# Performance work log

Hardware: AMD Instinct MI355X
Metric: run time of the kernel (lower is better)

Reference implementation:

```python
import jax, jax.numpy as jnp
import numpy as np

# --- placement constants (mirror init_kwargs) ---
N = 500_000           # total nodes
M = 450_000           # movable nodes (first M)
NBX = 1024
NBY = 1024
XL = 0.0
YL = 0.0
BSX = 1.0
BSY = 1.0
K = 8                 # max bin span per axis for 'large' nodes (node size < 7*bin)


def setup_inputs() -> dict:
    key = jax.random.key(0)
    k1, k2, k3, k4, k5, k6 = jax.random.split(key, 6)
    # node centers strictly inside the die so large-node windows stay in range
    px = jax.random.uniform(k1, (N,), jnp.float32, 4.0, 1020.0)
    py = jax.random.uniform(k2, (N,), jnp.float32, 4.0, 1020.0)
    pos = jnp.concatenate([px, py])                      # [2N]
    potential_field = jax.random.normal(k3, (NBX, NBY), jnp.float32)
    rho_current = jax.random.uniform(k4, (NBX, NBY), jnp.float32, 0.1, 2.0)
    node_size_x = jax.random.uniform(k5, (N,), jnp.float32, 0.2, 6.0)
    node_size_y = jax.random.uniform(k6, (N,), jnp.float32, 0.2, 6.0)
    return {"pos": pos, "potential_field": potential_field,
            "rho_current": rho_current,
            "node_size_x": node_size_x, "node_size_y": node_size_y}


def _velocity_field(pot, hx, hy):
    # v = -grad(phi): 2nd-order central interior, 1st-order one-sided edges
    vx = -jnp.concatenate([(pot[1:2] - pot[0:1]) / hx,
                           (pot[2:] - pot[:-2]) / (2.0 * hx),
                           (pot[-1:] - pot[-2:-1]) / hx], axis=0)
    vy = -jnp.concatenate([(pot[:, 1:2] - pot[:, 0:1]) / hy,
                           (pot[:, 2:] - pot[:, :-2]) / (2.0 * hy),
                           (pot[:, -1:] - pot[:, -2:-1]) / hy], axis=1)
    return vx, vy


def _axis_window(center, size, lo, bs, nb):
    # per-node K-bin window of overlap lengths along one axis
    left = center - 0.5 * size
    right = center + 0.5 * size
    bmin = jnp.clip(jnp.floor((left - lo) / bs).astype(jnp.int32), 0, nb - 1)
    bmax = jnp.clip(jnp.floor((right - lo) / bs).astype(jnp.int32), 0, nb - 1)
    b = bmin[:, None] + jnp.arange(K, dtype=jnp.int32)        # [M,K]
    bin_left = lo + b.astype(jnp.float32) * bs
    ov = jnp.minimum(right[:, None], bin_left + bs) - jnp.maximum(left[:, None], bin_left)
    ov = jnp.where((b <= bmax[:, None]) & (ov > 0.0), ov, 0.0)
    return jnp.clip(b, 0, nb - 1), ov


def _interpolate_flux(pos, flux_x, flux_y, nsx, nsy):
    pos_x = pos[:N]
    pos_y = pos[N:]
    px = pos_x[:M]
    py = pos_y[:M]
    # --- bilinear path (small nodes) ---
    gx = (px - XL) / BSX
    gy = (py - YL) / BSY
    ix = jnp.clip(jnp.floor(gx).astype(jnp.int32), 0, NBX - 1)
    iy = jnp.clip(jnp.floor(gy).astype(jnp.int32), 0, NBY - 1)
    wx = jnp.clip(gx - ix.astype(jnp.float32), 0.0, 1.0)
    wy = jnp.clip(gy - iy.astype(jnp.float32), 0.0, 1.0)
    ix1 = jnp.clip(ix + 1, 0, NBX - 1)
    iy1 = jnp.clip(iy + 1, 0, NBY - 1)

    def bilerp(f):
        return ((1.0 - wx) * (1.0 - wy) * f[ix, iy] + wx * (1.0 - wy) * f[ix1, iy]
                + (1.0 - wx) * wy * f[ix, iy1] + wx * wy * f[ix1, iy1])

    bil_fx = bilerp(flux_x)
    bil_fy = bilerp(flux_y)
    # --- exact area-weighted path (large nodes), vectorized over K x K window ---
    w = nsx[:M]
    h = nsy[:M]
    bx, ox = _axis_window(px, w, XL, BSX, NBX)                # [M,K]
    by, oy = _axis_window(py, h, YL, BSY, NBY)                # [M,K]
    weights = ox[:, :, None] * oy[:, None, :]                 # [M,K,K] overlap areas
    fx_win = flux_x[bx[:, :, None], by[:, None, :]]           # [M,K,K]
    fy_win = flux_y[bx[:, :, None], by[:, None, :]]
    area = w * h
    safe_area = jnp.maximum(area, 1e-30)
    area_fx = jnp.where(area > 0.0, (fx_win * weights).sum((1, 2)) / safe_area, 0.0)
    area_fy = jnp.where(area > 0.0, (fy_win * weights).sum((1, 2)) / safe_area, 0.0)
    large = (w >= BSX) | (h >= BSY)
    gpx = jnp.where(large, area_fx, bil_fx)
    gpy = jnp.where(large, area_fy, bil_fy)
    grad_pos = jnp.zeros_like(pos)
    grad_pos = grad_pos.at[:M].set(gpx)
    grad_pos = grad_pos.at[N:N + M].set(gpy)
    return grad_pos


def reference(pos, potential_field, rho_current, node_size_x, node_size_y):
    vx, vy = _velocity_field(potential_field, BSX, BSY)
    bin_area = BSX * BSY
    energy = 0.5 * (rho_current * bin_area * (vx * vx + vy * vy)).sum().reshape(1)
    grad_pos = _interpolate_flux(pos, vx, vy, node_size_x, node_size_y)
    return energy, grad_pos
```

## Files before the change

### kernel.cpp

```cpp
#include <hip/hip_runtime.h>
#include <hip/hip_fp16.h>

#define NPART 500000
#define MPART 450000
#define NBXC 1024
#define NBYC 1024
#define KWIN 8

__global__ __launch_bounds__(256) void field_kernel(const float* __restrict__ pot,
                                                    const float* __restrict__ rho,
                                                    __half2* __restrict__ v,
                                                    float* __restrict__ partials) {
    const int idx = blockIdx.x * 256 + threadIdx.x;
    const int i = idx >> 10;
    const int j = idx & 1023;

    float a, b, scale;
    if (i == 0)            { a = pot[1 * NBYC + j];        b = pot[0 * NBYC + j];        scale = 1.0f; }
    else if (i == NBXC - 1){ a = pot[(NBXC-1) * NBYC + j]; b = pot[(NBXC-2) * NBYC + j]; scale = 1.0f; }
    else                   { a = pot[(i+1) * NBYC + j];    b = pot[(i-1) * NBYC + j];    scale = 0.5f; }
    const float vx = -(a - b) * scale;

    if (j == 0)            { a = pot[i * NBYC + 1];        b = pot[i * NBYC + 0];        scale = 1.0f; }
    else if (j == NBYC - 1){ a = pot[i * NBYC + NBYC-1];   b = pot[i * NBYC + NBYC-2];   scale = 1.0f; }
    else                   { a = pot[i * NBYC + j + 1];    b = pot[i * NBYC + j - 1];    scale = 0.5f; }
    const float vy = -(a - b) * scale;

    v[idx] = __floats2half2_rn(vx, vy);

    float e = rho[idx] * (vx * vx + vy * vy);
    #pragma unroll
    for (int off = 32; off > 0; off >>= 1) e += __shfl_down(e, off, 64);
    __shared__ float smem[4];
    const int lane = threadIdx.x & 63;
    const int wid  = threadIdx.x >> 6;
    if (lane == 0) smem[wid] = e;
    __syncthreads();
    if (threadIdx.x == 0) partials[blockIdx.x] = (smem[0] + smem[1]) + (smem[2] + smem[3]);
}

__global__ __launch_bounds__(1024) void reduce_kernel(const float* __restrict__ partials,
                                                      float* __restrict__ out) {
    const int t = threadIdx.x;
    float e = (partials[t] + partials[t + 1024]) + (partials[t + 2048] + partials[t + 3072]);
    #pragma unroll
    for (int off = 32; off > 0; off >>= 1) e += __shfl_down(e, off, 64);
    __shared__ float smem[16];
    const int lane = t & 63;
    const int wid  = t >> 6;
    if (lane == 0) smem[wid] = e;
    __syncthreads();
    if (t == 0) {
        float s = 0.0f;
        #pragma unroll
        for (int k = 0; k < 16; ++k) s += smem[k];
        out[0] = 0.5f * s;
    }
}

__global__ __launch_bounds__(256) void particle_kernel(const float* __restrict__ pos,
                                                       const float* __restrict__ nsx,
                                                       const float* __restrict__ nsy,
                                                       const __half2* __restrict__ v,
                                                       float* __restrict__ out) {
    const int i = blockIdx.x * 256 + threadIdx.x;
    if (i >= NPART) return;
    if (i >= MPART) {
        out[1 + i]         = 0.0f;
        out[1 + NPART + i] = 0.0f;
        return;
    }

    const float px = pos[i];
    const float py = pos[NPART + i];
    const float w  = nsx[i];
    const float h  = nsy[i];

    float gpx, gpy;
    const bool large = (w >= 1.0f) || (h >= 1.0f);
    if (!large) {
        int ix = min(max((int)floorf(px), 0), NBXC - 1);
        int iy = min(max((int)floorf(py), 0), NBYC - 1);
        const float wx = fminf(fmaxf(px - (float)ix, 0.0f), 1.0f);
        const float wy = fminf(fmaxf(py - (float)iy, 0.0f), 1.0f);
        const int ix1 = min(ix + 1, NBXC - 1);
        const int iy1 = min(iy + 1, NBYC - 1);
        const float2 f00 = __half22float2(v[ix  * NBYC + iy ]);
        const float2 f10 = __half22float2(v[ix1 * NBYC + iy ]);
        const float2 f01 = __half22float2(v[ix  * NBYC + iy1]);
        const float2 f11 = __half22float2(v[ix1 * NBYC + iy1]);
        const float w00 = (1.0f - wx) * (1.0f - wy);
        const float w10 = wx * (1.0f - wy);
        const float w01 = (1.0f - wx) * wy;
        const float w11 = wx * wy;
        gpx = w00 * f00.x + w10 * f10.x + w01 * f01.x + w11 * f11.x;
        gpy = w00 * f00.y + w10 * f10.y + w01 * f01.y + w11 * f11.y;
    } else {
        const float lx = px - 0.5f * w, rx = px + 0.5f * w;
        const float ly = py - 0.5f * h, ry = py + 0.5f * h;
        const int bminx = min(max((int)floorf(lx), 0), NBXC - 1);
        const int bmaxx = min(max((int)floorf(rx), 0), NBXC - 1);
        const int bminy = min(max((int)floorf(ly), 0), NBYC - 1);
        const int bmaxy = min(max((int)floorf(ry), 0), NBYC - 1);
        const int by0   = bminy & ~3;

        float oy[12];
        #pragma unroll
        for (int k = 0; k < 12; ++k) {
            const int b = by0 + k;
            const float bl = (float)b;
            float ov = fminf(ry, bl + 1.0f) - fmaxf(ly, bl);
            oy[k] = (b <= bmaxy && ov > 0.0f) ? ov : 0.0f;
        }

        float afx = 0.0f, afy = 0.0f;
        #pragma unroll
        for (int kx = 0; kx < KWIN; ++kx) {
            const int b = bminx + kx;
            const float bl = (float)b;
            float ov = fminf(rx, bl + 1.0f) - fmaxf(lx, bl);
            ov = (b <= bmaxx && ov > 0.0f) ? ov : 0.0f;
            if (ov == 0.0f) continue;
            const int bx = min(b, NBXC - 1);
            const float4* rp = reinterpret_cast<const float4*>(v + bx * NBYC + by0);
            float4 q0 = rp[0], q1 = rp[1], q2 = rp[2];
            const float* qs0 = &q0.x;
            const float* qs1 = &q1.x;
            const float* qs2 = &q2.x;
            float sx = 0.0f, sy = 0.0f;
            #pragma unroll
            for (int k = 0; k < 4; ++k) {
                const float2 f = __half22float2(__builtin_bit_cast(__half2, qs0[k]));
                sx += f.x * oy[k];
                sy += f.y * oy[k];
            }
            #pragma unroll
            for (int k = 0; k < 4; ++k) {
                const float2 f = __half22float2(__builtin_bit_cast(__half2, qs1[k]));
                sx += f.x * oy[4 + k];
                sy += f.y * oy[4 + k];
            }
            #pragma unroll
            for (int k = 0; k < 4; ++k) {
                const float2 f = __half22float2(__builtin_bit_cast(__half2, qs2[k]));
                sx += f.x * oy[8 + k];
                sy += f.y * oy[8 + k];
            }
            afx += sx * ov;
            afy += sy * ov;
        }
        const float inv = 1.0f / fmaxf(w * h, 1e-30f);
        gpx = afx * inv;
        gpy = afy * inv;
    }
    out[1 + i]         = gpx;
    out[1 + NPART + i] = gpy;
}

extern "C" void kernel_launch(void* const* d_in, const int* in_sizes, int n_in,
                              void* d_out, int out_size, void* d_ws, size_t ws_size,
                              hipStream_t stream) {
    const float* pos = (const float*)d_in[0];
    const float* pot = (const float*)d_in[1];
    const float* rho = (const float*)d_in[2];
    const float* nsx = (const float*)d_in[3];
    const float* nsy = (const float*)d_in[4];
    float* out = (float*)d_out;

    __half2* v      = (__half2*)d_ws;
    float* partials = (float*)((char*)d_ws + (size_t)NBXC * NBYC * sizeof(__half2));

    field_kernel<<<(NBXC * NBYC) / 256, 256, 0, stream>>>(pot, rho, v, partials);
    reduce_kernel<<<1, 1024, 0, stream>>>(partials, out);
    particle_kernel<<<(NPART + 255) / 256, 256, 0, stream>>>(pos, nsx, nsy, v, out);
}
```

Measured before the change: 33.65 us.

## Vectorize field kernel four-wide and fold energy reduction into particle kernel

Each field-kernel thread now handles four consecutive bins using float4 loads of the potential and rho rows and a single float4 store of the packed half2 velocities, cutting the thread count and partial sums by a factor of four. The separate reduce kernel is dropped; an extra block appended to the particle kernel sums the 1024 partials, saving one launch. In the large-node path the x-axis overlaps are precomputed and the per-column early-continue is removed, so all eight rows are loaded unconditionally. This trades more memory traffic for less divergence, and the y window start is clamped so the 12-wide reads stay in bounds.

```diff
diff --git a/kernel.cpp b/kernel.cpp
--- a/kernel.cpp
+++ b/kernel.cpp
@@ -6,29 +6,49 @@
 #define NBXC 1024
 #define NBYC 1024
 #define KWIN 8
+#define NBLK_PART 1954
+#define NPARTIALS 1024
 
 __global__ __launch_bounds__(256) void field_kernel(const float* __restrict__ pot,
                                                     const float* __restrict__ rho,
                                                     __half2* __restrict__ v,
                                                     float* __restrict__ partials) {
     const int idx = blockIdx.x * 256 + threadIdx.x;
-    const int i = idx >> 10;
-    const int j = idx & 1023;
+    const int i  = idx >> 8;
+    const int j4 = (idx & 255) << 2;
 
-    float a, b, scale;
-    if (i == 0)            { a = pot[1 * NBYC + j];        b = pot[0 * NBYC + j];        scale = 1.0f; }
-    else if (i == NBXC - 1){ a = pot[(NBXC-1) * NBYC + j]; b = pot[(NBXC-2) * NBYC + j]; scale = 1.0f; }
-    else                   { a = pot[(i+1) * NBYC + j];    b = pot[(i-1) * NBYC + j];    scale = 0.5f; }
-    const float vx = -(a - b) * scale;
+    const int ip = min(i + 1, NBXC - 1);
+    const int im = max(i - 1, 0);
+    const float sx = (ip - im == 2) ? 0.5f : 1.0f;
 
-    if (j == 0)            { a = pot[i * NBYC + 1];        b = pot[i * NBYC + 0];        scale = 1.0f; }
-    else if (j == NBYC - 1){ a = pot[i * NBYC + NBYC-1];   b = pot[i * NBYC + NBYC-2];   scale = 1.0f; }
-    else                   { a = pot[i * NBYC + j + 1];    b = pot[i * NBYC + j - 1];    scale = 0.5f; }
-    const float vy = -(a - b) * scale;
+    const float4 c  = *reinterpret_cast<const float4*>(pot + i  * NBYC + j4);
+    const float4 cu = *reinterpret_cast<const float4*>(pot + ip * NBYC + j4);
+    const float4 cd = *reinterpret_cast<const float4*>(pot + im * NBYC + j4);
+    const float  cl = pot[i * NBYC + max(j4 - 1, 0)];
+    const float  cr = pot[i * NBYC + min(j4 + 4, NBYC - 1)];
+    const float4 r4 = *reinterpret_cast<const float4*>(rho + i * NBYC + j4);
 
-    v[idx] = __floats2half2_rn(vx, vy);
+    const float vx0 = -(cu.x - cd.x) * sx;
+    const float vx1 = -(cu.y - cd.y) * sx;
+    const float vx2 = -(cu.z - cd.z) * sx;
+    const float vx3 = -(cu.w - cd.w) * sx;
 
-    float e = rho[idx] * (vx * vx + vy * vy);
+    const float vy0 = (j4 == 0)             ? -(c.y - c.x) : -(c.y - cl) * 0.5f;
+    const float vy1 = -(c.z - c.x) * 0.5f;
+    const float vy2 = -(c.w - c.y) * 0.5f;
+    const float vy3 = (j4 + 3 == NBYC - 1)  ? -(c.w - c.z) : -(cr - c.z) * 0.5f;
+
+    float4 st;
+    st.x = __builtin_bit_cast(float, __floats2half2_rn(vx0, vy0));
+    st.y = __builtin_bit_cast(float, __floats2half2_rn(vx1, vy1));
+    st.z = __builtin_bit_cast(float, __floats2half2_rn(vx2, vy2));
+    st.w = __builtin_bit_cast(float, __floats2half2_rn(vx3, vy3));
+    *reinterpret_cast<float4*>(v + i * NBYC + j4) = st;
+
+    float e = r4.x * (vx0 * vx0 + vy0 * vy0)
+            + r4.y * (vx1 * vx1 + vy1 * vy1)
+            + r4.z * (vx2 * vx2 + vy2 * vy2)
+            + r4.w * (vx3 * vx3 + vy3 * vy3);
     #pragma unroll
     for (int off = 32; off > 0; off >>= 1) e += __shfl_down(e, off, 64);
     __shared__ float smem[4];
@@ -39,30 +59,27 @@
     if (threadIdx.x == 0) partials[blockIdx.x] = (smem[0] + smem[1]) + (smem[2] + smem[3]);
 }
 
-__global__ __launch_bounds__(1024) void reduce_kernel(const float* __restrict__ partials,
-                                                      float* __restrict__ out) {
-    const int t = threadIdx.x;
-    float e = (partials[t] + partials[t + 1024]) + (partials[t + 2048] + partials[t + 3072]);
-    #pragma unroll
-    for (int off = 32; off > 0; off >>= 1) e += __shfl_down(e, off, 64);
-    __shared__ float smem[16];
-    const int lane = t & 63;
-    const int wid  = t >> 6;
-    if (lane == 0) smem[wid] = e;
-    __syncthreads();
-    if (t == 0) {
-        float s = 0.0f;
-        #pragma unroll
-        for (int k = 0; k < 16; ++k) s += smem[k];
-        out[0] = 0.5f * s;
-    }
-}
-
 __global__ __launch_bounds__(256) void particle_kernel(const float* __restrict__ pos,
                                                        const float* __restrict__ nsx,
                                                        const float* __restrict__ nsy,
                                                        const __half2* __restrict__ v,
+                                                       const float* __restrict__ partials,
                                                        float* __restrict__ out) {
+    __shared__ float smem[4];
+
+    if (blockIdx.x == NBLK_PART) {
+        const int t = threadIdx.x;
+        float e = (partials[t] + partials[t + 256]) + (partials[t + 512] + partials[t + 768]);
+        #pragma unroll
+        for (int off = 32; off > 0; off >>= 1) e += __shfl_down(e, off, 64);
+        const int lane = t & 63;
+        const int wid  = t >> 6;
+        if (lane == 0) smem[wid] = e;
+        __syncthreads();
+        if (t == 0) out[0] = 0.5f * ((smem[0] + smem[1]) + (smem[2] + smem[3]));
+        return;
+    }
+
     const int i = blockIdx.x * 256 + threadIdx.x;
     if (i >= NPART) return;
     if (i >= MPART) {
@@ -102,7 +119,7 @@
         const int bmaxx = min(max((int)floorf(rx), 0), NBXC - 1);
         const int bminy = min(max((int)floorf(ly), 0), NBYC - 1);
         const int bmaxy = min(max((int)floorf(ry), 0), NBYC - 1);
-        const int by0   = bminy & ~3;
+        const int by0 = min(bminy & ~3, NBYC - 12);
 
         float oy[12];
         #pragma unroll
@@ -112,16 +129,19 @@
             float ov = fminf(ry, bl + 1.0f) - fmaxf(ly, bl);
             oy[k] = (b <= bmaxy && ov > 0.0f) ? ov : 0.0f;
         }
+        float ox[KWIN];
+        #pragma unroll
+        for (int k = 0; k < KWIN; ++k) {
+            const int b = bminx + k;
+            const float bl = (float)b;
+            float ov = fminf(rx, bl + 1.0f) - fmaxf(lx, bl);
+            ox[k] = (b <= bmaxx && ov > 0.0f) ? ov : 0.0f;
+        }
 
         float afx = 0.0f, afy = 0.0f;
         #pragma unroll
         for (int kx = 0; kx < KWIN; ++kx) {
-            const int b = bminx + kx;
-            const float bl = (float)b;
-            float ov = fminf(rx, bl + 1.0f) - fmaxf(lx, bl);
-            ov = (b <= bmaxx && ov > 0.0f) ? ov : 0.0f;
-            if (ov == 0.0f) continue;
-            const int bx = min(b, NBXC - 1);
+            const int bx = min(bminx + kx, NBXC - 1);
             const float4* rp = reinterpret_cast<const float4*>(v + bx * NBYC + by0);
             float4 q0 = rp[0], q1 = rp[1], q2 = rp[2];
             const float* qs0 = &q0.x;
@@ -146,8 +166,8 @@
                 sx += f.x * oy[8 + k];
                 sy += f.y * oy[8 + k];
             }
-            afx += sx * ov;
-            afy += sy * ov;
+            afx += sx * ox[kx];
+            afy += sy * ox[kx];
         }
         const float inv = 1.0f / fmaxf(w * h, 1e-30f);
         gpx = afx * inv;
@@ -170,7 +190,6 @@
     __half2* v      = (__half2*)d_ws;
     float* partials = (float*)((char*)d_ws + (size_t)NBXC * NBYC * sizeof(__half2));
 
-    field_kernel<<<(NBXC * NBYC) / 256, 256, 0, stream>>>(pot, rho, v, partials);
-    reduce_kernel<<<1, 1024, 0, stream>>>(partials, out);
-    particle_kernel<<<(NPART + 255) / 256, 256, 0, stream>>>(pos, nsx, nsy, v, out);
+    field_kernel<<<(NBXC * NBYC / 4) / 256, 256, 0, stream>>>(pot, rho, v, partials);
+    particle_kernel<<<NBLK_PART + 1, 256, 0, stream>>>(pos, nsx, nsy, v, partials, out);
 }
```

Result: slower. 41.59 us (+23.6%).
